# Optimization experiments

Measured on AMD Instinct MI355X. Metric: run time of the kernel, lower is better.

Reference implementation:

```python
import jax, jax.numpy as jnp
import numpy as np
import math

NUM_HEADS = 16
HEAD_SIZE = 64
HIDDEN = NUM_HEADS * HEAD_SIZE
LN_EPS = 1e-12


def setup_inputs() -> dict:
    key = jax.random.key(0)
    ks = jax.random.split(key, 8)
    B, Lw, Le, H = 8, 512, 64, HIDDEN
    scale = 0.02
    return {
        "word_hidden_states": jax.random.normal(ks[0], (B, Lw, H), jnp.float32),
        "entity_hidden_states": jax.random.normal(ks[1], (B, Le, H), jnp.float32),
        "attention_mask": jnp.zeros((B, 1, 1, Lw + Le), jnp.float32),
        "Wq": jax.random.normal(ks[2], (H, H), jnp.float32) * scale,
        "bq": jnp.zeros((H,), jnp.float32),
        "Wk": jax.random.normal(ks[3], (H, H), jnp.float32) * scale,
        "bk": jnp.zeros((H,), jnp.float32),
        "Wv": jax.random.normal(ks[4], (H, H), jnp.float32) * scale,
        "bv": jnp.zeros((H,), jnp.float32),
        "Wo": jax.random.normal(ks[5], (H, H), jnp.float32) * scale,
        "bo": jnp.zeros((H,), jnp.float32),
        "ln_w": jnp.ones((H,), jnp.float32),
        "ln_b": jnp.zeros((H,), jnp.float32),
    }


def _layernorm(x, w, b):
    u = jnp.mean(x, axis=-1, keepdims=True)
    s = jnp.mean(jnp.square(x - u), axis=-1, keepdims=True)
    return w * ((x - u) / jnp.sqrt(s + LN_EPS)) + b


def reference(word_hidden_states, entity_hidden_states, attention_mask,
              Wq, bq, Wk, bk, Wv, bv, Wo, bo, ln_w, ln_b):
    B, Lw, H = word_hidden_states.shape
    x = jnp.concatenate([word_hidden_states, entity_hidden_states], axis=1)  # [B,S,H]
    S = x.shape[1]

    def heads(t):  # [B,S,H] -> [B,nh,S,hd]
        return t.reshape(B, S, NUM_HEADS, HEAD_SIZE).transpose(0, 2, 1, 3)

    q = heads(x @ Wq + bq)
    k = heads(x @ Wk + bk)
    v = heads(x @ Wv + bv)

    scores = jnp.einsum("bhqd,bhkd->bhqk", q, k) / math.sqrt(HEAD_SIZE)
    scores = scores + attention_mask  # additive mask, broadcast [B,1,1,S]
    probs = jax.nn.softmax(scores, axis=-1)
    ctx = jnp.einsum("bhqk,bhkd->bhqd", probs, v)
    ctx = ctx.transpose(0, 2, 1, 3).reshape(B, S, H)

    # SelfOutput (shared weights) applied per-stream; equivalent on concat since
    # residual is the concatenated input and LayerNorm is per-token.
    out = _layernorm(ctx @ Wo + bo + x, ln_w, ln_b)
    return out[:, :Lw, :], out[:, Lw:, :]
```

## Files before the change

kernel.cpp:

```cpp
#include <hip/hip_runtime.h>

#define NHEADS 16
#define HDIM   64
#define HID    1024
#define BATCH  8
#define LW     512
#define LE     64
#define SEQ    576
#define MTOT   (BATCH * SEQ)

typedef unsigned short u16;
typedef __bf16 bf16x8 __attribute__((ext_vector_type(8)));
typedef float  f32x4  __attribute__((ext_vector_type(4)));

__device__ __forceinline__ u16 f2bf(float f) {
  union { float f; unsigned int i; } x;
  x.f = f;
  unsigned int u = x.i;
  unsigned int r = (u + 0x7FFFu + ((u >> 16) & 1u)) >> 16;
  return (u16)r;
}
__device__ __forceinline__ unsigned int pk2(float a, float b) {
  return (unsigned int)f2bf(a) | ((unsigned int)f2bf(b) << 16);
}

__device__ __forceinline__ void gload16(const u16* g, u16* l) {
  __builtin_amdgcn_global_load_lds(
      (const __attribute__((address_space(1))) void*)g,
      (__attribute__((address_space(3))) void*)l, 16, 0, 0);
}

__global__ __launch_bounds__(256) void transp_k(
    const float* __restrict__ w0, const float* __restrict__ w1,
    const float* __restrict__ w2, const float* __restrict__ w3,
    u16* __restrict__ wt)
{
  __shared__ u16 tile[32][33];
  const float* src = (blockIdx.z == 0) ? w0 : (blockIdx.z == 1) ? w1
                   : (blockIdx.z == 2) ? w2 : w3;
  u16* dst = wt + (size_t)blockIdx.z * HID * HID;
  const int tx = threadIdx.x, ty = threadIdx.y;
  const int nx = blockIdx.x * 32;
  const int ky = blockIdx.y * 32;
#pragma unroll
  for (int j = 0; j < 4; ++j)
    tile[ty * 4 + j][tx] = f2bf(src[(size_t)(ky + ty * 4 + j) * HID + nx + tx]);
  __syncthreads();
#pragma unroll
  for (int j = 0; j < 4; ++j)
    dst[(size_t)(nx + ty * 4 + j) * HID + ky + tx] = tile[tx][ty * 4 + j];
}

__global__ __launch_bounds__(256) void xcvt_k(
    const float* __restrict__ word, const float* __restrict__ ent,
    u16* __restrict__ xb)
{
  const int row = blockIdx.x, tid = threadIdx.x;
  const int bb = row / SEQ, ss = row - bb * SEQ;
  const float* src = (ss < LW) ? word + (size_t)(bb * LW + ss) * HID
                               : ent  + (size_t)(bb * LE + (ss - LW)) * HID;
  float4 v = *(const float4*)(src + tid * 4);
  ushort4 o;
  o.x = f2bf(v.x); o.y = f2bf(v.y); o.z = f2bf(v.z); o.w = f2bf(v.w);
  *(ushort4*)(xb + (size_t)row * HID + tid * 4) = o;
}

__global__ __launch_bounds__(256) void qkv_gemm_k(
    const u16* __restrict__ xb, const u16* __restrict__ wt,
    const float* __restrict__ bq, const float* __restrict__ bk, const float* __restrict__ bv,
    u16* __restrict__ q_ws, u16* __restrict__ k_ws, u16* __restrict__ v_ws)
{
  __shared__ u16 sh[4 * 64 * 68];
  u16* As = sh;
  u16* Bs = sh + 4096;
  const int which = blockIdx.z;
  const u16* W = wt + (size_t)which * HID * HID;
  const float* bias = (which == 0) ? bq : (which == 1) ? bk : bv;
  const int m0 = blockIdx.x * 128, n0 = blockIdx.y * 128;
  const int tid = threadIdx.x, lane = tid & 63, wv = tid >> 6;
  const int lr = lane & 15, quad = lane >> 4;
  const int wm = (wv >> 1) * 64, wn = (wv & 1) * 64;
  const int srow = wv * 16 + (lane >> 2);
  const int gseg = ((lane & 3) ^ ((lane >> 4) & 3)) * 8;
  const int lseg = (lane & 3) * 8;
  const u16* ga0 = xb + (size_t)(m0 + srow) * HID + gseg;
  const u16* ga1 = ga0 + (size_t)64 * HID;
  const u16* gb0 = W + (size_t)(n0 + srow) * HID + gseg;
  const u16* gb1 = gb0 + (size_t)64 * HID;
  u16* la0 = As + srow * 32 + lseg;
  u16* la1 = la0 + 64 * 32;
  u16* lb0 = Bs + srow * 32 + lseg;
  u16* lb1 = lb0 + 64 * 32;
  const int fc = (quad ^ (lr >> 2)) * 8;

  const f32x4 fz = {0.f, 0.f, 0.f, 0.f};
  f32x4 acc[4][4];
#pragma unroll
  for (int mi = 0; mi < 4; ++mi)
#pragma unroll
    for (int ni = 0; ni < 4; ++ni) acc[mi][ni] = fz;

  for (int k0 = 0; k0 < HID; k0 += 32) {
    gload16(ga0 + k0, la0);
    gload16(ga1 + k0, la1);
    gload16(gb0 + k0, lb0);
    gload16(gb1 + k0, lb1);
    __syncthreads();
    bf16x8 af[4], bfr[4];
#pragma unroll
    for (int i = 0; i < 4; ++i) {
      af[i]  = *(const bf16x8*)(&As[(wm + i * 16 + lr) * 32 + fc]);
      bfr[i] = *(const bf16x8*)(&Bs[(wn + i * 16 + lr) * 32 + fc]);
    }
#pragma unroll
    for (int mi = 0; mi < 4; ++mi)
#pragma unroll
      for (int ni = 0; ni < 4; ++ni)
        acc[mi][ni] = __builtin_amdgcn_mfma_f32_16x16x32_bf16(af[mi], bfr[ni], acc[mi][ni], 0, 0, 0);
    __syncthreads();
  }

  u16* tb = sh + wv * (64 * 68);
  const int head = (n0 + wn) >> 6;
  const int mbase = m0 + wm;
  const int bb = mbase / SEQ;
  const int ssb = mbase - bb * SEQ;
  float bcol[4];
#pragma unroll
  for (int ni = 0; ni < 4; ++ni) bcol[ni] = bias[n0 + wn + ni * 16 + lr];

  if (which < 2) {
#pragma unroll
    for (int mi = 0; mi < 4; ++mi)
#pragma unroll
      for (int ni = 0; ni < 4; ++ni)
#pragma unroll
        for (int r = 0; r < 4; ++r)
          tb[(mi * 16 + quad * 4 + r) * 68 + ni * 16 + lr] = f2bf(acc[mi][ni][r] + bcol[ni]);
    u16* drow = (which == 0 ? q_ws : k_ws)
              + ((size_t)(bb * NHEADS + head) * SEQ + ssb) * HDIM;
#pragma unroll
    for (int i = 0; i < 8; ++i) {
      int rrow = i * 8 + (lane >> 3);
      int seg = lane & 7;
      bf16x8 v8 = *(const bf16x8*)(&tb[rrow * 68 + seg * 8]);
      *(bf16x8*)(drow + (size_t)rrow * HDIM + seg * 8) = v8;
    }
  } else {
#pragma unroll
    for (int mi = 0; mi < 4; ++mi)
#pragma unroll
      for (int ni = 0; ni < 4; ++ni)
#pragma unroll
        for (int r = 0; r < 4; ++r)
          tb[(ni * 16 + lr) * 68 + (mi >> 1) * 32 + quad * 8 + (mi & 1) * 4 + r]
              = f2bf(acc[mi][ni][r] + bcol[ni]);
    u16* dcol = v_ws + ((size_t)(bb * NHEADS + head) * HDIM) * SEQ + ssb;
#pragma unroll
    for (int i = 0; i < 8; ++i) {
      int d = i * 8 + (lane >> 3);
      int seg = lane & 7;
      bf16x8 v8 = *(const bf16x8*)(&tb[d * 68 + seg * 8]);
      *(bf16x8*)(dcol + (size_t)d * SEQ + seg * 8) = v8;
    }
  }
}

__global__ __launch_bounds__(256) void attn_k(
    const u16* __restrict__ q_ws, const u16* __restrict__ k_ws,
    const u16* __restrict__ v_ws, const float* __restrict__ mask,
    u16* __restrict__ ctxh)
{
  __shared__ u16 Ks[2][4096];
  __shared__ u16 Vs[2][4096];
  __shared__ float ms[576];
  const int bhx = blockIdx.x, qt = blockIdx.y;
  const int b = bhx >> 4, h = bhx & 15;
  const int tid = threadIdx.x, lane = tid & 63, wv = tid >> 6;
  const int lr = lane & 15, quad = lane >> 4;
  const int q0 = qt * 64 + wv * 16;
  const u16* kbh = k_ws + (size_t)bhx * SEQ * HDIM;
  const u16* vbh = v_ws + (size_t)bhx * HDIM * SEQ;
  const u16* qp  = q_ws + ((size_t)bhx * SEQ + q0) * HDIM;
  const float* mrow = mask + b * SEQ;

  if (tid < 144) *(float4*)(&ms[tid * 4]) = *(const float4*)(mrow + tid * 4);

  const int subrow = lane >> 3;
  const int gsw = (lane & 7) ^ subrow;

  bf16x8 qf[2];
  qf[0] = *(const bf16x8*)(qp + lr * HDIM + quad * 8);
  qf[1] = *(const bf16x8*)(qp + lr * HDIM + 32 + quad * 8);

  const f32x4 fz = {0.f, 0.f, 0.f, 0.f};
  f32x4 oa[4] = {fz, fz, fz, fz};
  f32x4 rsv = fz;
  const int fA = lr & 7;

#pragma unroll
  for (int j = 0; j < 2; ++j) {
    int row = (wv * 2 + j) * 8 + subrow;
    gload16(kbh + (size_t)row * HDIM + gsw * 8, &Ks[0][((wv * 2 + j) * 64 + lane) * 8]);
    gload16(vbh + (size_t)row * SEQ + gsw * 8,  &Vs[0][((wv * 2 + j) * 64 + lane) * 8]);
  }

  for (int ci = 0; ci < 9; ++ci) {
    const int cur = ci & 1;
    const int c = ci * 64;
    __syncthreads();
    if (ci + 1 < 9) {
      int cn = c + 64;
#pragma unroll
      for (int j = 0; j < 2; ++j) {
        int row = (wv * 2 + j) * 8 + subrow;
        gload16(kbh + ((size_t)(cn + row)) * HDIM + gsw * 8,
                &Ks[cur ^ 1][((wv * 2 + j) * 64 + lane) * 8]);
        gload16(vbh + (size_t)row * SEQ + cn + gsw * 8,
                &Vs[cur ^ 1][((wv * 2 + j) * 64 + lane) * 8]);
      }
    }
    f32x4 s[4] = {fz, fz, fz, fz};
#pragma unroll
    for (int ks = 0; ks < 2; ++ks)
#pragma unroll
      for (int t = 0; t < 4; ++t) {
        bf16x8 kf = *(const bf16x8*)(&Ks[cur][(t * 16 + lr) * 64 + (((ks * 4 + quad) ^ fA) * 8)]);
        s[t] = __builtin_amdgcn_mfma_f32_16x16x32_bf16(kf, qf[ks], s[t], 0, 0, 0);
      }
    unsigned int pk0[4], pk1[4];
#pragma unroll
    for (int t = 0; t < 4; ++t) {
      float4 mv = *(const float4*)(&ms[c + t * 16 + quad * 4]);
      s[t][0] = __expf(s[t][0] * 0.125f + mv.x);
      s[t][1] = __expf(s[t][1] * 0.125f + mv.y);
      s[t][2] = __expf(s[t][2] * 0.125f + mv.z);
      s[t][3] = __expf(s[t][3] * 0.125f + mv.w);
      rsv += s[t];
      pk0[t] = pk2(s[t][0], s[t][1]);
      pk1[t] = pk2(s[t][2], s[t][3]);
    }
#pragma unroll
    for (int ks = 0; ks < 2; ++ks) {
      union { unsigned int u[4]; bf16x8 v; } ap;
      ap.u[0] = pk0[ks * 2];     ap.u[1] = pk1[ks * 2];
      ap.u[2] = pk0[ks * 2 + 1]; ap.u[3] = pk1[ks * 2 + 1];
#pragma unroll
      for (int n = 0; n < 4; ++n) {
        bf16x8 vf = *(const bf16x8*)(&Vs[cur][(n * 16 + lr) * 64 + (((ks * 4 + quad) ^ fA) * 8)]);
        oa[n] = __builtin_amdgcn_mfma_f32_16x16x32_bf16(ap.v, vf, oa[n], 0, 0, 0);
      }
    }
  }

  float rl = rsv[0] + rsv[1] + rsv[2] + rsv[3];
  rl += __shfl_xor(rl, 16);
  rl += __shfl_xor(rl, 32);
  float inv = 1.0f / rl;
  float invr[4];
#pragma unroll
  for (int r = 0; r < 4; ++r) invr[r] = __shfl(inv, quad * 4 + r);

  u16* pw = (wv < 2) ? &Ks[1][wv * 2048] : &Vs[1][(wv - 2) * 2048];
#pragma unroll
  for (int n = 0; n < 4; ++n)
#pragma unroll
    for (int r = 0; r < 4; ++r)
      pw[(quad * 4 + r) * 68 + n * 16 + lr] = f2bf(oa[n][r] * invr[r]);
  const int token0 = b * SEQ + q0;
  u16* cb = ctxh + ((size_t)h * MTOT + token0) * HDIM;
#pragma unroll
  for (int i = 0; i < 2; ++i) {
    int row = lane & 15;
    int seg = (lane >> 4) + i * 4;
    bf16x8 v8 = *(const bf16x8*)(&pw[row * 68 + seg * 8]);
    *(bf16x8*)(cb + (size_t)row * HDIM + seg * 8) = v8;
  }
}

__global__ __launch_bounds__(256) void out_gemm_k(
    const u16* __restrict__ ctxh, const u16* __restrict__ wto,
    const float* __restrict__ bo,
    const float* __restrict__ word, const float* __restrict__ ent,
    float* __restrict__ y)
{
  __shared__ u16 As[64 * 32];
  __shared__ u16 Bs[128 * 32];
  const int m0 = blockIdx.x * 64, n0 = blockIdx.y * 128;
  const int tid = threadIdx.x, lane = tid & 63, wv = tid >> 6;
  const int lr = lane & 15, quad = lane >> 4;
  const int wm = (wv & 1) * 32, wn = (wv >> 1) * 64;
  const int srow = wv * 16 + (lane >> 2);
  const int gseg = ((lane & 3) ^ ((lane >> 4) & 3)) * 8;
  const int lseg = (lane & 3) * 8;
  u16* laA  = As + srow * 32 + lseg;
  u16* laB0 = Bs + srow * 32 + lseg;
  u16* laB1 = laB0 + 64 * 32;
  const u16* gb0 = wto + (size_t)(n0 + srow) * HID + gseg;
  const u16* gb1 = gb0 + (size_t)64 * HID;
  const int fc = (quad ^ (lr >> 2)) * 8;

  const f32x4 fz = {0.f, 0.f, 0.f, 0.f};
  f32x4 acc[2][4];
#pragma unroll
  for (int mi = 0; mi < 2; ++mi)
#pragma unroll
    for (int ni = 0; ni < 4; ++ni) acc[mi][ni] = fz;

  for (int k0 = 0; k0 < HID; k0 += 32) {
    const int hblk = k0 >> 6, koff = k0 & 63;
    gload16(ctxh + ((size_t)hblk * MTOT + (m0 + srow)) * HDIM + koff + gseg, laA);
    gload16(gb0 + k0, laB0);
    gload16(gb1 + k0, laB1);
    __syncthreads();
    bf16x8 af[2], bfr[4];
#pragma unroll
    for (int i = 0; i < 2; ++i)
      af[i] = *(const bf16x8*)(&As[(wm + i * 16 + lr) * 32 + fc]);
#pragma unroll
    for (int i = 0; i < 4; ++i)
      bfr[i] = *(const bf16x8*)(&Bs[(wn + i * 16 + lr) * 32 + fc]);
#pragma unroll
    for (int mi = 0; mi < 2; ++mi)
#pragma unroll
      for (int ni = 0; ni < 4; ++ni)
        acc[mi][ni] = __builtin_amdgcn_mfma_f32_16x16x32_bf16(af[mi], bfr[ni], acc[mi][ni], 0, 0, 0);
    __syncthreads();
  }

#pragma unroll
  for (int mi = 0; mi < 2; ++mi) {
    int rowb = m0 + wm + mi * 16 + quad * 4;
#pragma unroll
    for (int r = 0; r < 4; ++r) {
      int row = rowb + r;
      int bb = row / SEQ, ss = row - bb * SEQ;
      const float* res = (ss < LW) ? (word + (size_t)(bb * LW + ss) * HID)
                                   : (ent  + (size_t)(bb * LE + (ss - LW)) * HID);
#pragma unroll
      for (int ni = 0; ni < 4; ++ni) {
        int col = n0 + wn + ni * 16 + lr;
        y[(size_t)row * HID + col] = acc[mi][ni][r] + bo[col] + res[col];
      }
    }
  }
}

__global__ __launch_bounds__(256) void ln_k(
    const float* __restrict__ y, const float* __restrict__ lnw,
    const float* __restrict__ lnb, float* __restrict__ out)
{
  const int row = blockIdx.x;
  const int tid = threadIdx.x;
  __shared__ float ssum[4], sqq[4];

  const float* yr = y + (size_t)row * HID;
  float4 v = *(const float4*)(yr + tid * 4);
  float s = v.x + v.y + v.z + v.w;
  float q = v.x * v.x + v.y * v.y + v.z * v.z + v.w * v.w;
#pragma unroll
  for (int o = 32; o > 0; o >>= 1) { s += __shfl_xor(s, o); q += __shfl_xor(q, o); }
  if ((tid & 63) == 0) { ssum[tid >> 6] = s; sqq[tid >> 6] = q; }
  __syncthreads();
  s = ssum[0] + ssum[1] + ssum[2] + ssum[3];
  q = sqq[0] + sqq[1] + sqq[2] + sqq[3];
  float mean = s * (1.0f / HID);
  float var  = q * (1.0f / HID) - mean * mean;
  float rstd = rsqrtf(var + 1e-12f);

  int bb = row / SEQ, ss2 = row - bb * SEQ;
  float* dst = (ss2 < LW)
             ? out + (size_t)(bb * LW + ss2) * HID
             : out + (size_t)BATCH * LW * HID + (size_t)(bb * LE + (ss2 - LW)) * HID;

  float4 w4 = *(const float4*)(lnw + tid * 4);
  float4 b4 = *(const float4*)(lnb + tid * 4);
  float4 o4;
  o4.x = w4.x * (v.x - mean) * rstd + b4.x;
  o4.y = w4.y * (v.y - mean) * rstd + b4.y;
  o4.z = w4.z * (v.z - mean) * rstd + b4.z;
  o4.w = w4.w * (v.w - mean) * rstd + b4.w;
  *(float4*)(dst + tid * 4) = o4;
}

extern "C" void kernel_launch(void* const* d_in, const int* in_sizes, int n_in,
                              void* d_out, int out_size, void* d_ws, size_t ws_size,
                              hipStream_t stream) {
  const float* word = (const float*)d_in[0];
  const float* ent  = (const float*)d_in[1];
  const float* mask = (const float*)d_in[2];
  const float* Wq   = (const float*)d_in[3];
  const float* bq   = (const float*)d_in[4];
  const float* Wk   = (const float*)d_in[5];
  const float* bk   = (const float*)d_in[6];
  const float* Wv   = (const float*)d_in[7];
  const float* bv   = (const float*)d_in[8];
  const float* Wo   = (const float*)d_in[9];
  const float* bo   = (const float*)d_in[10];
  const float* lnw  = (const float*)d_in[11];
  const float* lnb  = (const float*)d_in[12];

  char* base = (char*)d_ws;
  u16*   wt   = (u16*)base;
  u16*   q_ws = (u16*)(base + (size_t)8 * 1024 * 1024);
  u16*   k_ws = q_ws + (size_t)MTOT * HID;
  u16*   v_ws = k_ws + (size_t)MTOT * HID;
  u16*   ctxh = v_ws + (size_t)MTOT * HID;
  char*  xy   = (char*)(ctxh + (size_t)MTOT * HID);
  u16*   xb   = (u16*)xy;
  float* y    = (float*)xy;

  hipLaunchKernelGGL(transp_k, dim3(32, 32, 4), dim3(32, 8), 0, stream,
                     Wq, Wk, Wv, Wo, wt);
  hipLaunchKernelGGL(xcvt_k, dim3(MTOT), dim3(256), 0, stream, word, ent, xb);
  hipLaunchKernelGGL(qkv_gemm_k, dim3(MTOT / 128, HID / 128, 3), dim3(256), 0, stream,
                     xb, wt, bq, bk, bv, q_ws, k_ws, v_ws);
  hipLaunchKernelGGL(attn_k, dim3(BATCH * NHEADS, SEQ / 64), dim3(256), 0, stream,
                     q_ws, k_ws, v_ws, mask, ctxh);
  hipLaunchKernelGGL(out_gemm_k, dim3(MTOT / 64, HID / 128), dim3(256), 0, stream,
                     ctxh, wt + (size_t)3 * HID * HID, bo, word, ent, y);
  hipLaunchKernelGGL(ln_k, dim3(MTOT), dim3(256), 0, stream,
                     y, lnw, lnb, (float*)d_out);
}
```

Measured before the change: 210.1 us.

## Double-buffer GEMM loads, merge prep kernels, enlarge out-GEMM tile, vectorize epilogue stores

Merges the weight transpose and input conversion kernels into one launch. Adds LDS double buffering with one barrier per k-step to the QKV and output GEMMs, so the next tile's global-to-LDS loads overlap the current MFMAs. Enlarges the output GEMM tile from 64x128 to 128x128. For Q/K it swaps the MFMA operands so each lane holds consecutive columns, allowing packed uint2 LDS writes with float4 bias loads in the epilogue. The bigger output tile halves the number of blocks for that GEMM, and the extra accumulators raise register pressure.

```diff
diff --git a/kernel.cpp b/kernel.cpp
--- a/kernel.cpp
+++ b/kernel.cpp
@@ -30,39 +30,39 @@
       (__attribute__((address_space(3))) void*)l, 16, 0, 0);
 }
 
-__global__ __launch_bounds__(256) void transp_k(
+__global__ __launch_bounds__(256) void prep_k(
     const float* __restrict__ w0, const float* __restrict__ w1,
     const float* __restrict__ w2, const float* __restrict__ w3,
-    u16* __restrict__ wt)
-{
-  __shared__ u16 tile[32][33];
-  const float* src = (blockIdx.z == 0) ? w0 : (blockIdx.z == 1) ? w1
-                   : (blockIdx.z == 2) ? w2 : w3;
-  u16* dst = wt + (size_t)blockIdx.z * HID * HID;
-  const int tx = threadIdx.x, ty = threadIdx.y;
-  const int nx = blockIdx.x * 32;
-  const int ky = blockIdx.y * 32;
-#pragma unroll
-  for (int j = 0; j < 4; ++j)
-    tile[ty * 4 + j][tx] = f2bf(src[(size_t)(ky + ty * 4 + j) * HID + nx + tx]);
-  __syncthreads();
-#pragma unroll
-  for (int j = 0; j < 4; ++j)
-    dst[(size_t)(nx + ty * 4 + j) * HID + ky + tx] = tile[tx][ty * 4 + j];
-}
-
-__global__ __launch_bounds__(256) void xcvt_k(
+    u16* __restrict__ wt,
     const float* __restrict__ word, const float* __restrict__ ent,
     u16* __restrict__ xb)
 {
-  const int row = blockIdx.x, tid = threadIdx.x;
-  const int bb = row / SEQ, ss = row - bb * SEQ;
-  const float* src = (ss < LW) ? word + (size_t)(bb * LW + ss) * HID
-                               : ent  + (size_t)(bb * LE + (ss - LW)) * HID;
-  float4 v = *(const float4*)(src + tid * 4);
-  ushort4 o;
-  o.x = f2bf(v.x); o.y = f2bf(v.y); o.z = f2bf(v.z); o.w = f2bf(v.w);
-  *(ushort4*)(xb + (size_t)row * HID + tid * 4) = o;
+  const int bid = blockIdx.x, tid = threadIdx.x;
+  if (bid < 4096) {
+    __shared__ u16 tile[32][33];
+    const int z = bid >> 10, rem = bid & 1023;
+    const int bx = rem & 31, by = rem >> 5;
+    const float* src = (z == 0) ? w0 : (z == 1) ? w1 : (z == 2) ? w2 : w3;
+    u16* dst = wt + (size_t)z * HID * HID;
+    const int tx = tid & 31, ty = tid >> 5;
+    const int nx = bx * 32, ky = by * 32;
+#pragma unroll
+    for (int j = 0; j < 4; ++j)
+      tile[ty * 4 + j][tx] = f2bf(src[(size_t)(ky + ty * 4 + j) * HID + nx + tx]);
+    __syncthreads();
+#pragma unroll
+    for (int j = 0; j < 4; ++j)
+      dst[(size_t)(nx + ty * 4 + j) * HID + ky + tx] = tile[tx][ty * 4 + j];
+  } else {
+    const int row = bid - 4096;
+    const int bb = row / SEQ, ss = row - bb * SEQ;
+    const float* src = (ss < LW) ? word + (size_t)(bb * LW + ss) * HID
+                                 : ent  + (size_t)(bb * LE + (ss - LW)) * HID;
+    float4 v = *(const float4*)(src + tid * 4);
+    ushort4 o;
+    o.x = f2bf(v.x); o.y = f2bf(v.y); o.z = f2bf(v.z); o.w = f2bf(v.w);
+    *(ushort4*)(xb + (size_t)row * HID + tid * 4) = o;
+  }
 }
 
 __global__ __launch_bounds__(256) void qkv_gemm_k(
@@ -71,8 +71,6 @@
     u16* __restrict__ q_ws, u16* __restrict__ k_ws, u16* __restrict__ v_ws)
 {
   __shared__ u16 sh[4 * 64 * 68];
-  u16* As = sh;
-  u16* Bs = sh + 4096;
   const int which = blockIdx.z;
   const u16* W = wt + (size_t)which * HID * HID;
   const float* bias = (which == 0) ? bq : (which == 1) ? bk : bv;
@@ -83,60 +81,78 @@
   const int srow = wv * 16 + (lane >> 2);
   const int gseg = ((lane & 3) ^ ((lane >> 4) & 3)) * 8;
   const int lseg = (lane & 3) * 8;
-  const u16* ga0 = xb + (size_t)(m0 + srow) * HID + gseg;
-  const u16* ga1 = ga0 + (size_t)64 * HID;
-  const u16* gb0 = W + (size_t)(n0 + srow) * HID + gseg;
-  const u16* gb1 = gb0 + (size_t)64 * HID;
-  u16* la0 = As + srow * 32 + lseg;
-  u16* la1 = la0 + 64 * 32;
-  u16* lb0 = Bs + srow * 32 + lseg;
-  u16* lb1 = lb0 + 64 * 32;
+  const u16* gA = xb + (size_t)(m0 + srow) * HID + gseg;
+  const u16* gB = W + (size_t)(n0 + srow) * HID + gseg;
   const int fc = (quad ^ (lr >> 2)) * 8;
 
   const f32x4 fz = {0.f, 0.f, 0.f, 0.f};
   f32x4 acc[4][4];
 #pragma unroll
-  for (int mi = 0; mi < 4; ++mi)
-#pragma unroll
-    for (int ni = 0; ni < 4; ++ni) acc[mi][ni] = fz;
-
-  for (int k0 = 0; k0 < HID; k0 += 32) {
-    gload16(ga0 + k0, la0);
-    gload16(ga1 + k0, la1);
-    gload16(gb0 + k0, lb0);
-    gload16(gb1 + k0, lb1);
+  for (int a = 0; a < 4; ++a)
+#pragma unroll
+    for (int b = 0; b < 4; ++b) acc[a][b] = fz;
+
+  {
+    u16* As = sh; u16* Bs = sh + 4096;
+    gload16(gA, As + srow * 32 + lseg);
+    gload16(gA + (size_t)64 * HID, As + 2048 + srow * 32 + lseg);
+    gload16(gB, Bs + srow * 32 + lseg);
+    gload16(gB + (size_t)64 * HID, Bs + 2048 + srow * 32 + lseg);
+  }
+  for (int ki = 0; ki < 32; ++ki) {
+    const int cur = ki & 1;
     __syncthreads();
+    if (ki + 1 < 32) {
+      const int k0 = (ki + 1) * 32;
+      u16* As = sh + (cur ^ 1) * 8192; u16* Bs = As + 4096;
+      gload16(gA + k0, As + srow * 32 + lseg);
+      gload16(gA + (size_t)64 * HID + k0, As + 2048 + srow * 32 + lseg);
+      gload16(gB + k0, Bs + srow * 32 + lseg);
+      gload16(gB + (size_t)64 * HID + k0, Bs + 2048 + srow * 32 + lseg);
+    }
+    u16* As = sh + cur * 8192; u16* Bs = As + 4096;
     bf16x8 af[4], bfr[4];
 #pragma unroll
     for (int i = 0; i < 4; ++i) {
       af[i]  = *(const bf16x8*)(&As[(wm + i * 16 + lr) * 32 + fc]);
       bfr[i] = *(const bf16x8*)(&Bs[(wn + i * 16 + lr) * 32 + fc]);
     }
-#pragma unroll
-    for (int mi = 0; mi < 4; ++mi)
-#pragma unroll
-      for (int ni = 0; ni < 4; ++ni)
-        acc[mi][ni] = __builtin_amdgcn_mfma_f32_16x16x32_bf16(af[mi], bfr[ni], acc[mi][ni], 0, 0, 0);
-    __syncthreads();
-  }
+    if (which < 2) {
+#pragma unroll
+      for (int a = 0; a < 4; ++a)
+#pragma unroll
+        for (int b = 0; b < 4; ++b)
+          acc[a][b] = __builtin_amdgcn_mfma_f32_16x16x32_bf16(bfr[a], af[b], acc[a][b], 0, 0, 0);
+    } else {
+#pragma unroll
+      for (int a = 0; a < 4; ++a)
+#pragma unroll
+        for (int b = 0; b < 4; ++b)
+          acc[a][b] = __builtin_amdgcn_mfma_f32_16x16x32_bf16(af[a], bfr[b], acc[a][b], 0, 0, 0);
+    }
+  }
+  __syncthreads();
 
   u16* tb = sh + wv * (64 * 68);
   const int head = (n0 + wn) >> 6;
   const int mbase = m0 + wm;
   const int bb = mbase / SEQ;
   const int ssb = mbase - bb * SEQ;
-  float bcol[4];
-#pragma unroll
-  for (int ni = 0; ni < 4; ++ni) bcol[ni] = bias[n0 + wn + ni * 16 + lr];
 
   if (which < 2) {
+    float4 bias4[4];
+#pragma unroll
+    for (int ni = 0; ni < 4; ++ni)
+      bias4[ni] = *(const float4*)(bias + n0 + wn + ni * 16 + quad * 4);
 #pragma unroll
     for (int mi = 0; mi < 4; ++mi)
 #pragma unroll
-      for (int ni = 0; ni < 4; ++ni)
-#pragma unroll
-        for (int r = 0; r < 4; ++r)
-          tb[(mi * 16 + quad * 4 + r) * 68 + ni * 16 + lr] = f2bf(acc[mi][ni][r] + bcol[ni]);
+      for (int ni = 0; ni < 4; ++ni) {
+        uint2 w2v;
+        w2v.x = pk2(acc[ni][mi][0] + bias4[ni].x, acc[ni][mi][1] + bias4[ni].y);
+        w2v.y = pk2(acc[ni][mi][2] + bias4[ni].z, acc[ni][mi][3] + bias4[ni].w);
+        *(uint2*)(&tb[(mi * 16 + lr) * 68 + ni * 16 + quad * 4]) = w2v;
+      }
     u16* drow = (which == 0 ? q_ws : k_ws)
               + ((size_t)(bb * NHEADS + head) * SEQ + ssb) * HDIM;
 #pragma unroll
@@ -147,14 +163,18 @@
       *(bf16x8*)(drow + (size_t)rrow * HDIM + seg * 8) = v8;
     }
   } else {
+    float bcol[4];
+#pragma unroll
+    for (int ni = 0; ni < 4; ++ni) bcol[ni] = bias[n0 + wn + ni * 16 + lr];
 #pragma unroll
     for (int mi = 0; mi < 4; ++mi)
 #pragma unroll
-      for (int ni = 0; ni < 4; ++ni)
-#pragma unroll
-        for (int r = 0; r < 4; ++r)
-          tb[(ni * 16 + lr) * 68 + (mi >> 1) * 32 + quad * 8 + (mi & 1) * 4 + r]
-              = f2bf(acc[mi][ni][r] + bcol[ni]);
+      for (int ni = 0; ni < 4; ++ni) {
+        uint2 w2v;
+        w2v.x = pk2(acc[mi][ni][0] + bcol[ni], acc[mi][ni][1] + bcol[ni]);
+        w2v.y = pk2(acc[mi][ni][2] + bcol[ni], acc[mi][ni][3] + bcol[ni]);
+        *(uint2*)(&tb[(ni * 16 + lr) * 68 + (mi >> 1) * 32 + quad * 8 + (mi & 1) * 4]) = w2v;
+      }
     u16* dcol = v_ws + ((size_t)(bb * NHEADS + head) * HDIM) * SEQ + ssb;
 #pragma unroll
     for (int i = 0; i < 8; ++i) {
@@ -284,52 +304,59 @@
     const float* __restrict__ word, const float* __restrict__ ent,
     float* __restrict__ y)
 {
-  __shared__ u16 As[64 * 32];
-  __shared__ u16 Bs[128 * 32];
-  const int m0 = blockIdx.x * 64, n0 = blockIdx.y * 128;
+  __shared__ u16 sh[16384];
+  const int m0 = blockIdx.x * 128, n0 = blockIdx.y * 128;
   const int tid = threadIdx.x, lane = tid & 63, wv = tid >> 6;
   const int lr = lane & 15, quad = lane >> 4;
-  const int wm = (wv & 1) * 32, wn = (wv >> 1) * 64;
+  const int wm = (wv >> 1) * 64, wn = (wv & 1) * 64;
   const int srow = wv * 16 + (lane >> 2);
   const int gseg = ((lane & 3) ^ ((lane >> 4) & 3)) * 8;
   const int lseg = (lane & 3) * 8;
-  u16* laA  = As + srow * 32 + lseg;
-  u16* laB0 = Bs + srow * 32 + lseg;
-  u16* laB1 = laB0 + 64 * 32;
-  const u16* gb0 = wto + (size_t)(n0 + srow) * HID + gseg;
-  const u16* gb1 = gb0 + (size_t)64 * HID;
+  const u16* gB = wto + (size_t)(n0 + srow) * HID + gseg;
   const int fc = (quad ^ (lr >> 2)) * 8;
 
   const f32x4 fz = {0.f, 0.f, 0.f, 0.f};
-  f32x4 acc[2][4];
-#pragma unroll
-  for (int mi = 0; mi < 2; ++mi)
+  f32x4 acc[4][4];
+#pragma unroll
+  for (int mi = 0; mi < 4; ++mi)
 #pragma unroll
     for (int ni = 0; ni < 4; ++ni) acc[mi][ni] = fz;
 
-  for (int k0 = 0; k0 < HID; k0 += 32) {
-    const int hblk = k0 >> 6, koff = k0 & 63;
-    gload16(ctxh + ((size_t)hblk * MTOT + (m0 + srow)) * HDIM + koff + gseg, laA);
-    gload16(gb0 + k0, laB0);
-    gload16(gb1 + k0, laB1);
+  {
+    u16* As = sh; u16* Bs = sh + 4096;
+    gload16(ctxh + ((size_t)0 * MTOT + (m0 + srow)) * HDIM + 0 + gseg, As + srow * 32 + lseg);
+    gload16(ctxh + ((size_t)0 * MTOT + (m0 + 64 + srow)) * HDIM + 0 + gseg, As + 2048 + srow * 32 + lseg);
+    gload16(gB, Bs + srow * 32 + lseg);
+    gload16(gB + (size_t)64 * HID, Bs + 2048 + srow * 32 + lseg);
+  }
+  for (int ki = 0; ki < 32; ++ki) {
+    const int cur = ki & 1;
     __syncthreads();
-    bf16x8 af[2], bfr[4];
-#pragma unroll
-    for (int i = 0; i < 2; ++i)
-      af[i] = *(const bf16x8*)(&As[(wm + i * 16 + lr) * 32 + fc]);
-#pragma unroll
-    for (int i = 0; i < 4; ++i)
+    if (ki + 1 < 32) {
+      const int k0 = (ki + 1) * 32;
+      const int hblk = k0 >> 6, koff = k0 & 63;
+      u16* As = sh + (cur ^ 1) * 8192; u16* Bs = As + 4096;
+      gload16(ctxh + ((size_t)hblk * MTOT + (m0 + srow)) * HDIM + koff + gseg, As + srow * 32 + lseg);
+      gload16(ctxh + ((size_t)hblk * MTOT + (m0 + 64 + srow)) * HDIM + koff + gseg, As + 2048 + srow * 32 + lseg);
+      gload16(gB + k0, Bs + srow * 32 + lseg);
+      gload16(gB + (size_t)64 * HID + k0, Bs + 2048 + srow * 32 + lseg);
+    }
+    u16* As = sh + cur * 8192; u16* Bs = As + 4096;
+    bf16x8 af[4], bfr[4];
+#pragma unroll
+    for (int i = 0; i < 4; ++i) {
+      af[i]  = *(const bf16x8*)(&As[(wm + i * 16 + lr) * 32 + fc]);
       bfr[i] = *(const bf16x8*)(&Bs[(wn + i * 16 + lr) * 32 + fc]);
-#pragma unroll
-    for (int mi = 0; mi < 2; ++mi)
+    }
+#pragma unroll
+    for (int mi = 0; mi < 4; ++mi)
 #pragma unroll
       for (int ni = 0; ni < 4; ++ni)
         acc[mi][ni] = __builtin_amdgcn_mfma_f32_16x16x32_bf16(af[mi], bfr[ni], acc[mi][ni], 0, 0, 0);
-    __syncthreads();
-  }
-
-#pragma unroll
-  for (int mi = 0; mi < 2; ++mi) {
+  }
+
+#pragma unroll
+  for (int mi = 0; mi < 4; ++mi) {
     int rowb = m0 + wm + mi * 16 + quad * 4;
 #pragma unroll
     for (int r = 0; r < 4; ++r) {
@@ -410,14 +437,13 @@
   u16*   xb   = (u16*)xy;
   float* y    = (float*)xy;
 
-  hipLaunchKernelGGL(transp_k, dim3(32, 32, 4), dim3(32, 8), 0, stream,
-                     Wq, Wk, Wv, Wo, wt);
-  hipLaunchKernelGGL(xcvt_k, dim3(MTOT), dim3(256), 0, stream, word, ent, xb);
+  hipLaunchKernelGGL(prep_k, dim3(4096 + MTOT), dim3(256), 0, stream,
+                     Wq, Wk, Wv, Wo, wt, word, ent, xb);
   hipLaunchKernelGGL(qkv_gemm_k, dim3(MTOT / 128, HID / 128, 3), dim3(256), 0, stream,
                      xb, wt, bq, bk, bv, q_ws, k_ws, v_ws);
   hipLaunchKernelGGL(attn_k, dim3(BATCH * NHEADS, SEQ / 64), dim3(256), 0, stream,
                      q_ws, k_ws, v_ws, mask, ctxh);
-  hipLaunchKernelGGL(out_gemm_k, dim3(MTOT / 64, HID / 128), dim3(256), 0, stream,
+  hipLaunchKernelGGL(out_gemm_k, dim3(MTOT / 128, HID / 128), dim3(256), 0, stream,
                      ctxh, wt + (size_t)3 * HID * HID, bo, word, ent, y);
   hipLaunchKernelGGL(ln_k, dim3(MTOT), dim3(256), 0, stream,
                      y, lnw, lnb, (float*)d_out);
```

Result: faster. 203.6 us (-3.1%).
